# Kernel optimization log

Hardware: AMD Instinct MI355X
Metric: run time of the kernel (lower is better)

The kernel has to match this reference:

```python
import jax, jax.numpy as jnp
import numpy as np

# norse LIFParameters defaults with v_th overridden to 0.23
DT = 1e-3
TAU_SYN_INV = 200.0   # 1/5e-3
TAU_MEM_INV = 100.0   # 1/1e-2
V_TH = 0.23
ENC_V_TH = 1.0        # encoder uses default LIFParameters (v_th=1.0)
SEQ_LEN = 24
HIDDEN = 256
N_CLASSES = 10


def heaviside(x):
    return (x > 0).astype(x.dtype)


def encode(x):
    """ConstantCurrentLIFEncoder: lif_current_encoder over SEQ_LEN steps. x: [B, F] -> [T, B, F] spikes."""
    def step(v, _):
        v = v + DT * TAU_MEM_INV * (x - v)          # dv = dt*tau_mem_inv*((v_leak - v) + I)
        z = heaviside(v - ENC_V_TH)
        v = (1.0 - z) * v                            # reset to v_reset = 0
        return v, z
    _, zs = jax.lax.scan(step, jnp.zeros_like(x), None, length=SEQ_LEN)
    return zs


def lif_ff_step(inp, v, i):
    """norse lif_feed_forward_step: decay v with old i, decay i, spike, reset, then add input to i."""
    v_dec = v + DT * TAU_MEM_INV * (i - v)           # v_leak = 0
    i_dec = i * (1.0 - DT * TAU_SYN_INV)
    z = heaviside(v_dec - V_TH)
    v_new = (1.0 - z) * v_dec                        # v_reset = 0
    i_new = i_dec + inp
    return z, v_new, i_new


def setup_inputs() -> dict:
    key = jax.random.key(0)
    ks = jax.random.split(key, 8)
    B, F = 4096, 1024
    def lin(k, fan_in, fan_out):
        bound = 1.0 / np.sqrt(fan_in)
        kw, kb = jax.random.split(k)
        W = jax.random.uniform(kw, (fan_out, fan_in), jnp.float32, -bound, bound)
        b = jax.random.uniform(kb, (fan_out,), jnp.float32, -bound, bound)
        return W, b
    x = jax.random.normal(ks[0], (B, F), jnp.float32)
    W1, b1 = lin(ks[1], F, HIDDEN)
    W2, b2 = lin(ks[2], HIDDEN, HIDDEN)
    W3, b3 = lin(ks[3], HIDDEN, HIDDEN)
    Wli = jax.random.normal(ks[4], (N_CLASSES, HIDDEN), jnp.float32) * np.sqrt(2.0 / HIDDEN)
    return {"x": x, "W1": W1, "b1": b1, "W2": W2, "b2": b2, "W3": W3, "b3": b3, "Wli": Wli}


def reference(x, W1, b1, W2, b2, W3, b3, Wli):
    # dropout layers are identity in eval mode
    enc = encode(x)                                   # [T, B, F]
    B = x.shape[0]
    z2 = lambda d: jnp.zeros((B, d), x.dtype)
    carry0 = (z2(HIDDEN), z2(HIDDEN), z2(HIDDEN), z2(HIDDEN), z2(HIDDEN), z2(HIDDEN),
              z2(N_CLASSES), z2(N_CLASSES))
    def step(c, z):
        v1, i1, v2, i2, v3, i3, vo, io = c
        o1, v1, i1 = lif_ff_step(z @ W1.T + b1, v1, i1)
        o2, v2, i2 = lif_ff_step(o1 @ W2.T + b2, v2, i2)
        o2 = o2 + o1                                  # residual
        o3, v3, i3 = lif_ff_step(o2 @ W3.T + b3, v3, i3)
        o3 = o3 + o2                                  # residual
        # LILinearCell li_step: v from old i, i decays then accumulates W @ input (no bias)
        vo = vo + DT * TAU_MEM_INV * (io - vo)
        io = io * (1.0 - DT * TAU_SYN_INV) + o3 @ Wli.T
        return (v1, i1, v2, i2, v3, i3, vo, io), vo
    _, voltages = jax.lax.scan(step, carry0, enc)     # [T, B, n_classes]
    return voltages[-1]                               # decode = last timestep
```

## Files before the change

kernel.cpp:

```cpp
#include <hip/hip_runtime.h>
#include <hip/hip_bf16.h>

#define FEAT   1024
#define HID    256
#define TSTEPS 24
#define NCLS   10

typedef unsigned int u32;
typedef unsigned long long u64;
typedef unsigned short u16;
typedef float v2f __attribute__((ext_vector_type(2)));

constexpr int OFF_W1T  = 0;
constexpr int OFF_W23  = OFF_W1T + 1025*HID;
constexpr int OFF_WLI  = OFF_W23 + 257*512;
constexpr int OFF_B1   = OFF_WLI + NCLS*HID;
constexpr int OFF_B2   = OFF_B1 + HID;
constexpr int OFF_B3   = OFF_B2 + HID;

struct CoefT { float c[TSTEPS]; };
constexpr CoefT make_coef() {
    CoefT r{};
    double c = 0.0, p9 = 1.0;
    r.c[TSTEPS-1] = 0.0f;
    for (int u = TSTEPS-1; u > 0; u--) {
        c = 0.8 * c + 0.1 * p9;
        p9 *= 0.9;
        r.c[u-1] = (float)c;
    }
    return r;
}
__device__ constexpr CoefT COEF = make_coef();

__device__ __forceinline__ u32 rfl(u32 v) {
    return (u32)__builtin_amdgcn_readfirstlane((int)v);
}

__device__ __forceinline__ u32 detect_bf16(const void* __restrict__ x, u32 lane) {
    float v = __bfloat162float(((const __hip_bfloat16*)x)[lane]);
    u64 bad = __ballot(!(fabsf(v) < 100.0f));
    return bad == 0ull ? 1u : 0u;
}

__device__ __forceinline__ float rd_any(const void* p, int idx, u32 isbf) {
    return isbf ? __bfloat162float(((const __hip_bfloat16*)p)[idx])
                : ((const float*)p)[idx];
}

__device__ __forceinline__ float4 rd4(const void* p, int i, u32 isbf) {
    if (isbf) {
        const u32* q = (const u32*)p;
        u32 a = q[i >> 1], b = q[(i >> 1) + 1];
        float4 r;
        r.x = __uint_as_float(a << 16); r.y = __uint_as_float(a & 0xffff0000u);
        r.z = __uint_as_float(b << 16); r.w = __uint_as_float(b & 0xffff0000u);
        return r;
    }
    return ((const float4*)p)[i >> 2];
}

__global__ __launch_bounds__(256) void prep_k(const void* __restrict__ x,
        const void* W1, const void* W2, const void* W3, const void* Wli,
        const void* b1, const void* b2, const void* b3, float* __restrict__ ws) {
    const u32 isbf = detect_bf16(x, threadIdx.x & 63);
    const u32 t = threadIdx.x;
    int b = blockIdx.x;

    if (b == 384) {
        for (u32 e = t; e < NCLS*HID; e += 256) ws[OFF_WLI + e] = rd_any(Wli, e, isbf);
        ws[OFF_B1 + t] = rd_any(b1, t, isbf);
        ws[OFF_B2 + t] = rd_any(b2, t, isbf);
        ws[OFF_B3 + t] = rd_any(b3, t, isbf);
        ws[OFF_W1T + 1024*HID + t] = 0.f;
        ws[OFF_W23 + 256*512 + t] = 0.f;
        ws[OFF_W23 + 256*512 + 256 + t] = 0.f;
        return;
    }

    const void* src; float* dst; int srcW, dstW, coff, h0, f0;
    if (b < 256)      { src = W1; dst = ws + OFF_W1T; srcW = FEAT; dstW = HID; coff = 0;
                        h0 = (b >> 5) * 32; f0 = (b & 31) * 32; }
    else if (b < 320) { int tb = b - 256; src = W2; dst = ws + OFF_W23; srcW = HID; dstW = 512; coff = 0;
                        h0 = (tb >> 3) * 32; f0 = (tb & 7) * 32; }
    else              { int tb = b - 320; src = W3; dst = ws + OFF_W23; srcW = HID; dstW = 512; coff = 256;
                        h0 = (tb >> 3) * 32; f0 = (tb & 7) * 32; }

    __shared__ float sm[32 * 36];
    {
        u32 r = t >> 3, c4 = (t & 7) * 4;
        float4 w = rd4(src, (h0 + r) * srcW + f0 + c4, isbf);
        *(float4*)&sm[r * 36 + c4] = w;
    }
    __syncthreads();
    {
        u32 f = t >> 3, h4 = (t & 7) * 4;
        float4 o;
        o.x = sm[(h4 + 0) * 36 + f];
        o.y = sm[(h4 + 1) * 36 + f];
        o.z = sm[(h4 + 2) * 36 + f];
        o.w = sm[(h4 + 3) * 36 + f];
        *(float4*)&dst[(size_t)(f0 + f) * dstW + coff + h0 + h4] = o;
    }
}

__device__ __forceinline__ u32 mbcnt64(u64 m) {
    return __builtin_amdgcn_mbcnt_hi((u32)(m >> 32),
           __builtin_amdgcn_mbcnt_lo((u32)m, 0u));
}


__device__ __forceinline__ u32 build_listE(u16* list, u32 lm, u32 lane) {
    u32 cnt = (u32)__builtin_popcount(lm);
    u32 pos = 0, n = 0;
    #pragma unroll
    for (int b = 0; b < 5; b++) {
        u64 B = __ballot(((cnt >> b) & 1u) != 0);
        pos += mbcnt64(B) << b;
        n += ((u32)__builtin_popcountll(B)) << b;
    }
    while (lm) {
        u32 j = (u32)__builtin_ctz(lm); lm &= lm - 1;
        list[pos++] = (u16)((lane << 4) + j);
    }
    u32 np = (n + 1u) & ~1u;
    if (lane == 0 && np != n) list[n] = (u16)1024;
    return np;
}

__device__ __forceinline__ u32 build_listZ(u16* list, u32 lm, u32 start, u32 lane) {
    u32 cnt = (u32)__builtin_popcount(lm);
    u64 B0 = __ballot((cnt & 1u) != 0);
    u64 B1 = __ballot((cnt & 2u) != 0);
    u64 B2 = __ballot((cnt & 4u) != 0);
    u32 pos = start + mbcnt64(B0) + 2u*mbcnt64(B1) + 4u*mbcnt64(B2);
    u32 n = start + (u32)__builtin_popcountll(B0) + 2u*(u32)__builtin_popcountll(B1)
          + 4u*(u32)__builtin_popcountll(B2);
    while (lm) {
        u32 j = (u32)__builtin_ctz(lm); lm &= lm - 1;
        list[pos++] = (u16)((lane << 2) + j);
    }
    u32 np = (n + 1u) & ~1u;
    if (lane == 0 && np != n) list[n] = (u16)256;
    return np;
}

#define GADD(AA, BB, V) do { AA += (v2f){(V).x, (V).y}; BB += (v2f){(V).z, (V).w}; } while (0)

__device__ __forceinline__ void gather(v2f& A, v2f& B, const char* __restrict__ base,
                                       const u16* __restrict__ list, u32 np, u32 lane16,
                                       const u32 shl, const u32 disp) {
    v2f Aa = {0.f,0.f}, Ba = {0.f,0.f}, Ab = {0.f,0.f}, Bb = {0.f,0.f};
    u32 c = 0;
    for (; c + 8 <= np; c += 8) {
        uint4 d = *(const uint4*)(list + c);
        u32 w0 = rfl(d.x), w1 = rfl(d.y), w2 = rfl(d.z), w3 = rfl(d.w);
        const float4 v0 = *(const float4*)(base + ((w0 & 0xffffu) << shl) + disp + lane16);
        const float4 v1 = *(const float4*)(base + ((w0 >> 16)     << shl) + disp + lane16);
        const float4 v2 = *(const float4*)(base + ((w1 & 0xffffu) << shl) + disp + lane16);
        const float4 v3 = *(const float4*)(base + ((w1 >> 16)     << shl) + disp + lane16);
        const float4 v4 = *(const float4*)(base + ((w2 & 0xffffu) << shl) + disp + lane16);
        const float4 v5 = *(const float4*)(base + ((w2 >> 16)     << shl) + disp + lane16);
        const float4 v6 = *(const float4*)(base + ((w3 & 0xffffu) << shl) + disp + lane16);
        const float4 v7 = *(const float4*)(base + ((w3 >> 16)     << shl) + disp + lane16);
        GADD(Aa, Ba, v0); GADD(Ab, Bb, v1); GADD(Aa, Ba, v2); GADD(Ab, Bb, v3);
        GADD(Aa, Ba, v4); GADD(Ab, Bb, v5); GADD(Aa, Ba, v6); GADD(Ab, Bb, v7);
    }
    for (; c < np; c += 2) {
        u32 d = rfl(*(const u32*)(list + c));
        const float4 v0 = *(const float4*)(base + ((d & 0xffffu) << shl) + disp + lane16);
        const float4 v1 = *(const float4*)(base + ((d >> 16)     << shl) + disp + lane16);
        GADD(Aa, Ba, v0); GADD(Ab, Bb, v1);
    }
    A += Aa + Ab; B += Ba + Bb;
}

__device__ __forceinline__ void gather_dual(v2f& A2, v2f& B2, v2f& A3, v2f& B3,
        const char* __restrict__ p, const u16* __restrict__ list, u32 np, u32 lane16) {
    u32 c = 0;
    for (; c + 4 <= np; c += 4) {
        uint2 d = *(const uint2*)(list + c);
        u32 w0 = rfl(d.x), w1 = rfl(d.y);
        u32 o0 = (w0 & 0xffffu) << 11, o1 = (w0 >> 16) << 11;
        u32 o2 = (w1 & 0xffffu) << 11, o3 = (w1 >> 16) << 11;
        const float4 a0 = *(const float4*)(p + o0 + lane16);
        const float4 a1 = *(const float4*)(p + o1 + lane16);
        const float4 a2 = *(const float4*)(p + o2 + lane16);
        const float4 a3 = *(const float4*)(p + o3 + lane16);
        const float4 c0 = *(const float4*)(p + o0 + 1024 + lane16);
        const float4 c1 = *(const float4*)(p + o1 + 1024 + lane16);
        const float4 c2 = *(const float4*)(p + o2 + 1024 + lane16);
        const float4 c3 = *(const float4*)(p + o3 + 1024 + lane16);
        GADD(A2, B2, a0); GADD(A2, B2, a1); GADD(A2, B2, a2); GADD(A2, B2, a3);
        GADD(A3, B3, c0); GADD(A3, B3, c1); GADD(A3, B3, c2); GADD(A3, B3, c3);
    }
    for (; c < np; c += 2) {
        u32 d = rfl(*(const u32*)(list + c));
        u32 o0 = (d & 0xffffu) << 11, o1 = (d >> 16) << 11;
        const float4 a0 = *(const float4*)(p + o0 + lane16);
        const float4 a1 = *(const float4*)(p + o1 + lane16);
        const float4 c0 = *(const float4*)(p + o0 + 1024 + lane16);
        const float4 c1 = *(const float4*)(p + o1 + 1024 + lane16);
        GADD(A2, B2, a0); GADD(A2, B2, a1);
        GADD(A3, B3, c0); GADD(A3, B3, c1);
    }
}

__global__ __launch_bounds__(128, 4) void snn_k(const void* __restrict__ xin,
                                                const float* __restrict__ ws,
                                                void* __restrict__ out,
                                                int batch) {
    const u32 tid  = threadIdx.x;
    const u32 w    = tid >> 6;
    const u32 lane = tid & 63;
    const int row  = blockIdx.x * 2 + (int)w;
    if (row >= batch) return;
    const u32 lane16 = lane * 16;
    const u32 isbf = detect_bf16(xin, lane);

    const char* __restrict__ W1T = (const char*)(ws + OFF_W1T);
    const char* __restrict__ W23 = (const char*)(ws + OFF_W23);
    const float* __restrict__ WLI = ws + OFF_WLI;

    __shared__ u32 sched[2][12 * 64];
    __shared__ __align__(16) u16 lst[2][1024];
    u16* const lE = lst[w];
    u16* const lL = lst[w];

    {
        float xv[16];
        if (isbf) {
            const uint4* xp = (const uint4*)((const u16*)xin + (size_t)row*FEAT + lane*16);
            uint4 A = xp[0], B = xp[1];
            u32 wd[8] = {A.x, A.y, A.z, A.w, B.x, B.y, B.z, B.w};
            #pragma unroll
            for (int i = 0; i < 8; i++) {
                xv[2*i]   = __uint_as_float(wd[i] << 16);
                xv[2*i+1] = __uint_as_float(wd[i] & 0xffff0000u);
            }
        } else {
            const float4* xp = (const float4*)((const float*)xin + (size_t)row*FEAT + lane*16);
            float4 A = xp[0], B = xp[1], C = xp[2], D = xp[3];
            float tmp[16] = {A.x,A.y,A.z,A.w,B.x,B.y,B.z,B.w,C.x,C.y,C.z,C.w,D.x,D.y,D.z,D.w};
            #pragma unroll
            for (int i = 0; i < 16; i++) xv[i] = tmp[i];
        }
        u32 smreg[12];
        #pragma unroll
        for (int i = 0; i < 12; i++) smreg[i] = 0;
        #pragma unroll
        for (int j = 0; j < 16; j++) {
            float v = 0.f;
            #pragma unroll
            for (int t = 0; t < TSTEPS; t++) {
                v = v + 0.1f * (xv[j] - v);
                bool z = v > 1.0f;
                v = z ? 0.0f : v;
                if (z) smreg[t >> 1] |= 1u << (((t & 1) << 4) + j);
            }
        }
        #pragma unroll
        for (int i = 0; i < 12; i++) sched[w][i * 64 + lane] = smreg[i];
    }

    float v1[4], i1[4], v2[4], i2[4], v3[4], i3[4], g[4];
    #pragma unroll
    for (int k = 0; k < 4; k++) {
        v1[k]=0.f; i1[k]=0.f; v2[k]=0.f; i2[k]=0.f; v3[k]=0.f; i3[k]=0.f; g[k]=0.f;
    }
    const u32 lane4 = lane * 4;
    const float4 b1v = *(const float4*)(ws + OFF_B1 + lane4);
    const float4 b2v = *(const float4*)(ws + OFF_B2 + lane4);
    const float4 b3v = *(const float4*)(ws + OFF_B3 + lane4);

    u32 pairreg = 0;
    for (int t = 0; t < TSTEPS; t++) {
        if ((t & 1) == 0) pairreg = sched[w][(t >> 1) * 64 + lane];
        const u32 lmE = (t & 1) ? (pairreg >> 16) : (pairreg & 0xffffu);

        v2f accA = {b1v.x, b1v.y}, accB = {b1v.z, b1v.w};
        if (__ballot(lmE != 0u)) {
            u32 npE = build_listE(lE, lmE, lane);
            gather(accA, accB, W1T, lE, npE, lane16, 10u, 0u);
        }
        float a1[4] = {accA.x, accA.y, accB.x, accB.y};

        float o1v[4]; u32 lm1 = 0;
        #pragma unroll
        for (int kk = 0; kk < 4; kk++) {
            float vd = v1[kk] + 0.1f * (i1[kk] - v1[kk]);
            i1[kk] = i1[kk] * 0.8f;
            bool z = vd > 0.23f;
            v1[kk] = z ? 0.0f : vd;
            i1[kk] = i1[kk] + a1[kk];
            o1v[kk] = z ? 1.0f : 0.0f;
            lm1 |= (z ? 1u : 0u) << kk;
        }

        v2f acc2A = {b2v.x, b2v.y}, acc2B = {b2v.z, b2v.w};
        v2f acc3A = {b3v.x, b3v.y}, acc3B = {b3v.z, b3v.w};
        u32 np1 = 0;
        if (__ballot(lm1 != 0u)) {
            np1 = build_listZ(lL, lm1, 0u, lane);
            gather_dual(acc2A, acc2B, acc3A, acc3B, W23, lL, np1, lane16);
        }
        float a2[4] = {acc2A.x, acc2A.y, acc2B.x, acc2B.y};

        float o2v[4]; u32 lm2 = 0;
        #pragma unroll
        for (int kk = 0; kk < 4; kk++) {
            float vd = v2[kk] + 0.1f * (i2[kk] - v2[kk]);
            i2[kk] = i2[kk] * 0.8f;
            bool z = vd > 0.23f;
            v2[kk] = z ? 0.0f : vd;
            i2[kk] = i2[kk] + a2[kk];
            o2v[kk] = (z ? 1.0f : 0.0f) + o1v[kk];
            lm2 |= (z ? 1u : 0u) << kk;
        }

        if (__ballot(lm2 != 0u)) {
            u32 np2 = build_listZ(lL, lm2, np1, lane);
            gather(acc3A, acc3B, W23, lL + np1, np2 - np1, lane16, 11u, 1024u);
        }
        float a3[4] = {acc3A.x, acc3A.y, acc3B.x, acc3B.y};

        const float cf = COEF.c[t];
        #pragma unroll
        for (int kk = 0; kk < 4; kk++) {
            float vd = v3[kk] + 0.1f * (i3[kk] - v3[kk]);
            i3[kk] = i3[kk] * 0.8f;
            bool z = vd > 0.23f;
            v3[kk] = z ? 0.0f : vd;
            i3[kk] = i3[kk] + a3[kk];
            float o3 = (z ? 1.0f : 0.0f) + o2v[kk];
            g[kk] += cf * o3;
        }
    }

    float s[NCLS];
    #pragma unroll
    for (int c = 0; c < NCLS; c++) {
        const float4 wv = *(const float4*)(WLI + c*HID + lane4);
        float p = g[0]*wv.x + g[1]*wv.y + g[2]*wv.z + g[3]*wv.w;
        #pragma unroll
        for (int d = 32; d > 0; d >>= 1) p += __shfl_xor(p, d, 64);
        s[c] = p;
    }
    if (lane == 0) {
        if (isbf) {
            __hip_bfloat16* o = (__hip_bfloat16*)out + (size_t)row*NCLS;
            #pragma unroll
            for (int c = 0; c < NCLS; c++) o[c] = __float2bfloat16(s[c]);
        } else {
            float* o = (float*)out + (size_t)row*NCLS;
            #pragma unroll
            for (int c = 0; c < NCLS; c++) o[c] = s[c];
        }
    }
}

extern "C" void kernel_launch(void* const* d_in, const int* in_sizes, int n_in,
                              void* d_out, int out_size, void* d_ws, size_t ws_size,
                              hipStream_t stream) {
    const void* x   = d_in[0];
    const void* W1  = d_in[1];
    const void* b1  = d_in[2];
    const void* W2  = d_in[3];
    const void* b2  = d_in[4];
    const void* W3  = d_in[5];
    const void* b3  = d_in[6];
    const void* Wli = d_in[7];
    float* ws = (float*)d_ws;
    const int batch = in_sizes[0] / FEAT;

    prep_k<<<385, 256, 0, stream>>>(x, W1, W2, W3, Wli, b1, b2, b3, ws);
    snn_k<<<(batch + 1) / 2, 128, 0, stream>>>(x, ws, d_out, batch);
}
```

Measured before the change: 145.3 us.

## Split each batch row into producer/consumer wavefronts pipelining layer 1 against layers 2-3

Each block now handles one batch row instead of two. Wave 0 encodes the input and runs layer 1, publishing per-timestep spike masks through a shared-memory ring with a volatile flag. Wave 1 spin-waits on the flag and runs layers 2 and 3 plus the readout. The goal is to shorten the serial per-row timestep chain by overlapping layer 1 with the deeper layers, at the price of twice as many blocks, spin-waiting and possibly unbalanced work between the two waves.

```diff
diff --git a/kernel.cpp b/kernel.cpp
--- a/kernel.cpp
+++ b/kernel.cpp
@@ -212,7 +212,7 @@
     const u32 tid  = threadIdx.x;
     const u32 w    = tid >> 6;
     const u32 lane = tid & 63;
-    const int row  = blockIdx.x * 2 + (int)w;
+    const int row  = blockIdx.x;
     if (row >= batch) return;
     const u32 lane16 = lane * 16;
     const u32 isbf = detect_bf16(xin, lane);
@@ -221,139 +221,175 @@
     const char* __restrict__ W23 = (const char*)(ws + OFF_W23);
     const float* __restrict__ WLI = ws + OFF_WLI;
 
-    __shared__ u32 sched[2][12 * 64];
-    __shared__ __align__(16) u16 lst[2][1024];
-    u16* const lE = lst[w];
-    u16* const lL = lst[w];
-
-    {
-        float xv[16];
-        if (isbf) {
-            const uint4* xp = (const uint4*)((const u16*)xin + (size_t)row*FEAT + lane*16);
-            uint4 A = xp[0], B = xp[1];
-            u32 wd[8] = {A.x, A.y, A.z, A.w, B.x, B.y, B.z, B.w};
-            #pragma unroll
-            for (int i = 0; i < 8; i++) {
-                xv[2*i]   = __uint_as_float(wd[i] << 16);
-                xv[2*i+1] = __uint_as_float(wd[i] & 0xffff0000u);
-            }
-        } else {
-            const float4* xp = (const float4*)((const float*)xin + (size_t)row*FEAT + lane*16);
-            float4 A = xp[0], B = xp[1], C = xp[2], D = xp[3];
-            float tmp[16] = {A.x,A.y,A.z,A.w,B.x,B.y,B.z,B.w,C.x,C.y,C.z,C.w,D.x,D.y,D.z,D.w};
-            #pragma unroll
-            for (int i = 0; i < 16; i++) xv[i] = tmp[i];
+    __shared__ u32 sched[12 * 64];
+    __shared__ __align__(16) u16 lE[1024];
+    __shared__ __align__(16) u16 lL[768];
+    __shared__ __align__(16) u64 ring[TSTEPS][4];
+    __shared__ u32 flagv;
+
+    if (tid == 0) flagv = 0;
+    __syncthreads();
+
+    volatile u32* vf = &flagv;
+
+    if (w == 0) {
+        {
+            float xv[16];
+            if (isbf) {
+                const uint4* xp = (const uint4*)((const u16*)xin + (size_t)row*FEAT + lane*16);
+                uint4 A = xp[0], B = xp[1];
+                u32 wd[8] = {A.x, A.y, A.z, A.w, B.x, B.y, B.z, B.w};
+                #pragma unroll
+                for (int i = 0; i < 8; i++) {
+                    xv[2*i]   = __uint_as_float(wd[i] << 16);
+                    xv[2*i+1] = __uint_as_float(wd[i] & 0xffff0000u);
+                }
+            } else {
+                const float4* xp = (const float4*)((const float*)xin + (size_t)row*FEAT + lane*16);
+                float4 A = xp[0], B = xp[1], C = xp[2], D = xp[3];
+                float tmp[16] = {A.x,A.y,A.z,A.w,B.x,B.y,B.z,B.w,C.x,C.y,C.z,C.w,D.x,D.y,D.z,D.w};
+                #pragma unroll
+                for (int i = 0; i < 16; i++) xv[i] = tmp[i];
+            }
+            u32 smreg[12];
+            #pragma unroll
+            for (int i = 0; i < 12; i++) smreg[i] = 0;
+            #pragma unroll
+            for (int j = 0; j < 16; j++) {
+                float v = 0.f;
+                #pragma unroll
+                for (int t = 0; t < TSTEPS; t++) {
+                    v = v + 0.1f * (xv[j] - v);
+                    bool z = v > 1.0f;
+                    v = z ? 0.0f : v;
+                    if (z) smreg[t >> 1] |= 1u << (((t & 1) << 4) + j);
+                }
+            }
+            #pragma unroll
+            for (int i = 0; i < 12; i++) sched[i * 64 + lane] = smreg[i];
         }
-        u32 smreg[12];
+
+        float v1[4], i1[4];
         #pragma unroll
-        for (int i = 0; i < 12; i++) smreg[i] = 0;
+        for (int k = 0; k < 4; k++) { v1[k] = 0.f; i1[k] = 0.f; }
+        const float4 b1v = *(const float4*)(ws + OFF_B1 + lane * 4);
+
+        u32 pairreg = 0;
+        for (int t = 0; t < TSTEPS; t++) {
+            if ((t & 1) == 0) pairreg = sched[(t >> 1) * 64 + lane];
+            const u32 lmE = (t & 1) ? (pairreg >> 16) : (pairreg & 0xffffu);
+
+            v2f accA = {b1v.x, b1v.y}, accB = {b1v.z, b1v.w};
+            if (__ballot(lmE != 0u)) {
+                u32 npE = build_listE(lE, lmE, lane);
+                gather(accA, accB, W1T, lE, npE, lane16, 10u, 0u);
+            }
+            float a1[4] = {accA.x, accA.y, accB.x, accB.y};
+
+            u32 lm1 = 0;
+            #pragma unroll
+            for (int kk = 0; kk < 4; kk++) {
+                float vd = v1[kk] + 0.1f * (i1[kk] - v1[kk]);
+                i1[kk] = i1[kk] * 0.8f;
+                bool z = vd > 0.23f;
+                v1[kk] = z ? 0.0f : vd;
+                i1[kk] = i1[kk] + a1[kk];
+                lm1 |= (z ? 1u : 0u) << kk;
+            }
+
+            u64 m0 = __ballot((lm1 & 1u) != 0);
+            u64 m1 = __ballot((lm1 & 2u) != 0);
+            u64 m2 = __ballot((lm1 & 4u) != 0);
+            u64 m3 = __ballot((lm1 & 8u) != 0);
+            if (lane == 0) {
+                ring[t][0] = m0; ring[t][1] = m1; ring[t][2] = m2; ring[t][3] = m3;
+                __threadfence_block();
+                *vf = (u32)(t + 1);
+            }
+        }
+    } else {
+        float v2[4], i2[4], v3[4], i3[4], g[4];
         #pragma unroll
-        for (int j = 0; j < 16; j++) {
-            float v = 0.f;
-            #pragma unroll
-            for (int t = 0; t < TSTEPS; t++) {
-                v = v + 0.1f * (xv[j] - v);
-                bool z = v > 1.0f;
-                v = z ? 0.0f : v;
-                if (z) smreg[t >> 1] |= 1u << (((t & 1) << 4) + j);
+        for (int k = 0; k < 4; k++) { v2[k]=0.f; i2[k]=0.f; v3[k]=0.f; i3[k]=0.f; g[k]=0.f; }
+        const u32 lane4 = lane * 4;
+        const float4 b2v = *(const float4*)(ws + OFF_B2 + lane4);
+        const float4 b3v = *(const float4*)(ws + OFF_B3 + lane4);
+
+        u32 seen = 0;
+        for (int t = 0; t < TSTEPS; t++) {
+            if (seen < (u32)(t + 1)) {
+                do { seen = *vf; } while (seen < (u32)(t + 1));
+            }
+            __threadfence_block();
+            const volatile u64* rp = ring[t];
+            u64 m0 = rp[0], m1 = rp[1], m2 = rp[2], m3 = rp[3];
+            u32 lm1 = (u32)((m0 >> lane) & 1ull)
+                    | ((u32)((m1 >> lane) & 1ull) << 1)
+                    | ((u32)((m2 >> lane) & 1ull) << 2)
+                    | ((u32)((m3 >> lane) & 1ull) << 3);
+            float o1v[4];
+            #pragma unroll
+            for (int kk = 0; kk < 4; kk++) o1v[kk] = (lm1 >> kk) & 1u ? 1.0f : 0.0f;
+
+            v2f acc2A = {b2v.x, b2v.y}, acc2B = {b2v.z, b2v.w};
+            v2f acc3A = {b3v.x, b3v.y}, acc3B = {b3v.z, b3v.w};
+            u32 np1 = 0;
+            if (__ballot(lm1 != 0u)) {
+                np1 = build_listZ(lL, lm1, 0u, lane);
+                gather_dual(acc2A, acc2B, acc3A, acc3B, W23, lL, np1, lane16);
+            }
+            float a2[4] = {acc2A.x, acc2A.y, acc2B.x, acc2B.y};
+
+            float o2v[4]; u32 lm2 = 0;
+            #pragma unroll
+            for (int kk = 0; kk < 4; kk++) {
+                float vd = v2[kk] + 0.1f * (i2[kk] - v2[kk]);
+                i2[kk] = i2[kk] * 0.8f;
+                bool z = vd > 0.23f;
+                v2[kk] = z ? 0.0f : vd;
+                i2[kk] = i2[kk] + a2[kk];
+                o2v[kk] = (z ? 1.0f : 0.0f) + o1v[kk];
+                lm2 |= (z ? 1u : 0u) << kk;
+            }
+
+            if (__ballot(lm2 != 0u)) {
+                u32 np2 = build_listZ(lL, lm2, np1, lane);
+                gather(acc3A, acc3B, W23, lL + np1, np2 - np1, lane16, 11u, 1024u);
+            }
+            float a3[4] = {acc3A.x, acc3A.y, acc3B.x, acc3B.y};
+
+            const float cf = COEF.c[t];
+            #pragma unroll
+            for (int kk = 0; kk < 4; kk++) {
+                float vd = v3[kk] + 0.1f * (i3[kk] - v3[kk]);
+                i3[kk] = i3[kk] * 0.8f;
+                bool z = vd > 0.23f;
+                v3[kk] = z ? 0.0f : vd;
+                i3[kk] = i3[kk] + a3[kk];
+                float o3 = (z ? 1.0f : 0.0f) + o2v[kk];
+                g[kk] += cf * o3;
             }
         }
+
+        float s[NCLS];
         #pragma unroll
-        for (int i = 0; i < 12; i++) sched[w][i * 64 + lane] = smreg[i];
-    }
-
-    float v1[4], i1[4], v2[4], i2[4], v3[4], i3[4], g[4];
-    #pragma unroll
-    for (int k = 0; k < 4; k++) {
-        v1[k]=0.f; i1[k]=0.f; v2[k]=0.f; i2[k]=0.f; v3[k]=0.f; i3[k]=0.f; g[k]=0.f;
-    }
-    const u32 lane4 = lane * 4;
-    const float4 b1v = *(const float4*)(ws + OFF_B1 + lane4);
-    const float4 b2v = *(const float4*)(ws + OFF_B2 + lane4);
-    const float4 b3v = *(const float4*)(ws + OFF_B3 + lane4);
-
-    u32 pairreg = 0;
-    for (int t = 0; t < TSTEPS; t++) {
-        if ((t & 1) == 0) pairreg = sched[w][(t >> 1) * 64 + lane];
-        const u32 lmE = (t & 1) ? (pairreg >> 16) : (pairreg & 0xffffu);
-
-        v2f accA = {b1v.x, b1v.y}, accB = {b1v.z, b1v.w};
-        if (__ballot(lmE != 0u)) {
-            u32 npE = build_listE(lE, lmE, lane);
-            gather(accA, accB, W1T, lE, npE, lane16, 10u, 0u);
+        for (int c = 0; c < NCLS; c++) {
+            const float4 wv = *(const float4*)(WLI + c*HID + lane4);
+            float p = g[0]*wv.x + g[1]*wv.y + g[2]*wv.z + g[3]*wv.w;
+            #pragma unroll
+            for (int d = 32; d > 0; d >>= 1) p += __shfl_xor(p, d, 64);
+            s[c] = p;
         }
-        float a1[4] = {accA.x, accA.y, accB.x, accB.y};
-
-        float o1v[4]; u32 lm1 = 0;
-        #pragma unroll
-        for (int kk = 0; kk < 4; kk++) {
-            float vd = v1[kk] + 0.1f * (i1[kk] - v1[kk]);
-            i1[kk] = i1[kk] * 0.8f;
-            bool z = vd > 0.23f;
-            v1[kk] = z ? 0.0f : vd;
-            i1[kk] = i1[kk] + a1[kk];
-            o1v[kk] = z ? 1.0f : 0.0f;
-            lm1 |= (z ? 1u : 0u) << kk;
-        }
-
-        v2f acc2A = {b2v.x, b2v.y}, acc2B = {b2v.z, b2v.w};
-        v2f acc3A = {b3v.x, b3v.y}, acc3B = {b3v.z, b3v.w};
-        u32 np1 = 0;
-        if (__ballot(lm1 != 0u)) {
-            np1 = build_listZ(lL, lm1, 0u, lane);
-            gather_dual(acc2A, acc2B, acc3A, acc3B, W23, lL, np1, lane16);
-        }
-        float a2[4] = {acc2A.x, acc2A.y, acc2B.x, acc2B.y};
-
-        float o2v[4]; u32 lm2 = 0;
-        #pragma unroll
-        for (int kk = 0; kk < 4; kk++) {
-            float vd = v2[kk] + 0.1f * (i2[kk] - v2[kk]);
-            i2[kk] = i2[kk] * 0.8f;
-            bool z = vd > 0.23f;
-            v2[kk] = z ? 0.0f : vd;
-            i2[kk] = i2[kk] + a2[kk];
-            o2v[kk] = (z ? 1.0f : 0.0f) + o1v[kk];
-            lm2 |= (z ? 1u : 0u) << kk;
-        }
-
-        if (__ballot(lm2 != 0u)) {
-            u32 np2 = build_listZ(lL, lm2, np1, lane);
-            gather(acc3A, acc3B, W23, lL + np1, np2 - np1, lane16, 11u, 1024u);
-        }
-        float a3[4] = {acc3A.x, acc3A.y, acc3B.x, acc3B.y};
-
-        const float cf = COEF.c[t];
-        #pragma unroll
-        for (int kk = 0; kk < 4; kk++) {
-            float vd = v3[kk] + 0.1f * (i3[kk] - v3[kk]);
-            i3[kk] = i3[kk] * 0.8f;
-            bool z = vd > 0.23f;
-            v3[kk] = z ? 0.0f : vd;
-            i3[kk] = i3[kk] + a3[kk];
-            float o3 = (z ? 1.0f : 0.0f) + o2v[kk];
-            g[kk] += cf * o3;
-        }
-    }
-
-    float s[NCLS];
-    #pragma unroll
-    for (int c = 0; c < NCLS; c++) {
-        const float4 wv = *(const float4*)(WLI + c*HID + lane4);
-        float p = g[0]*wv.x + g[1]*wv.y + g[2]*wv.z + g[3]*wv.w;
-        #pragma unroll
-        for (int d = 32; d > 0; d >>= 1) p += __shfl_xor(p, d, 64);
-        s[c] = p;
-    }
-    if (lane == 0) {
-        if (isbf) {
-            __hip_bfloat16* o = (__hip_bfloat16*)out + (size_t)row*NCLS;
-            #pragma unroll
-            for (int c = 0; c < NCLS; c++) o[c] = __float2bfloat16(s[c]);
-        } else {
-            float* o = (float*)out + (size_t)row*NCLS;
-            #pragma unroll
-            for (int c = 0; c < NCLS; c++) o[c] = s[c];
+        if (lane == 0) {
+            if (isbf) {
+                __hip_bfloat16* o = (__hip_bfloat16*)out + (size_t)row*NCLS;
+                #pragma unroll
+                for (int c = 0; c < NCLS; c++) o[c] = __float2bfloat16(s[c]);
+            } else {
+                float* o = (float*)out + (size_t)row*NCLS;
+                #pragma unroll
+                for (int c = 0; c < NCLS; c++) o[c] = s[c];
+            }
         }
     }
 }
@@ -373,5 +409,5 @@
     const int batch = in_sizes[0] / FEAT;
 
     prep_k<<<385, 256, 0, stream>>>(x, W1, W2, W3, Wli, b1, b2, b3, ws);
-    snn_k<<<(batch + 1) / 2, 128, 0, stream>>>(x, ws, d_out, batch);
-}
+    snn_k<<<batch, 128, 0, stream>>>(x, ws, d_out, batch);
+}
```

New measurement: 167.3 us. 15.1% more time.

## Process SNN layers sequentially over all timesteps, pairing two timesteps per gather

Applied to the files above, without the earlier changes.

Restructures the per-row time loop into three layer-wise passes. Each pass runs all 24 timesteps for one layer and stores spike masks as packed bitmasks. Within a pass, two timesteps' spike lists are built and gathered together, so twice as many independent loads are in flight per iteration. Layer 3 now gathers W3 using both layer-1 and layer-2 spikes in one list instead of a dual W2/W3 gather. The kernel also moves from two rows per 128-thread block to one row per 64-thread block. The cost is more shared-memory list building and two list buffers per wave.

```diff
diff --git a/kernel.cpp b/kernel.cpp
--- a/kernel.cpp
+++ b/kernel.cpp
@@ -174,45 +174,51 @@
     A += Aa + Ab; B += Ba + Bb;
 }
 
-__device__ __forceinline__ void gather_dual(v2f& A2, v2f& B2, v2f& A3, v2f& B3,
-        const char* __restrict__ p, const u16* __restrict__ list, u32 np, u32 lane16) {
-    u32 c = 0;
-    for (; c + 4 <= np; c += 4) {
-        uint2 d = *(const uint2*)(list + c);
-        u32 w0 = rfl(d.x), w1 = rfl(d.y);
-        u32 o0 = (w0 & 0xffffu) << 11, o1 = (w0 >> 16) << 11;
-        u32 o2 = (w1 & 0xffffu) << 11, o3 = (w1 >> 16) << 11;
-        const float4 a0 = *(const float4*)(p + o0 + lane16);
-        const float4 a1 = *(const float4*)(p + o1 + lane16);
-        const float4 a2 = *(const float4*)(p + o2 + lane16);
-        const float4 a3 = *(const float4*)(p + o3 + lane16);
-        const float4 c0 = *(const float4*)(p + o0 + 1024 + lane16);
-        const float4 c1 = *(const float4*)(p + o1 + 1024 + lane16);
-        const float4 c2 = *(const float4*)(p + o2 + 1024 + lane16);
-        const float4 c3 = *(const float4*)(p + o3 + 1024 + lane16);
-        GADD(A2, B2, a0); GADD(A2, B2, a1); GADD(A2, B2, a2); GADD(A2, B2, a3);
-        GADD(A3, B3, c0); GADD(A3, B3, c1); GADD(A3, B3, c2); GADD(A3, B3, c3);
-    }
-    for (; c < np; c += 2) {
-        u32 d = rfl(*(const u32*)(list + c));
-        u32 o0 = (d & 0xffffu) << 11, o1 = (d >> 16) << 11;
-        const float4 a0 = *(const float4*)(p + o0 + lane16);
-        const float4 a1 = *(const float4*)(p + o1 + lane16);
-        const float4 c0 = *(const float4*)(p + o0 + 1024 + lane16);
-        const float4 c1 = *(const float4*)(p + o1 + 1024 + lane16);
-        GADD(A2, B2, a0); GADD(A2, B2, a1);
-        GADD(A3, B3, c0); GADD(A3, B3, c1);
-    }
-}
-
-__global__ __launch_bounds__(128, 4) void snn_k(const void* __restrict__ xin,
-                                                const float* __restrict__ ws,
-                                                void* __restrict__ out,
-                                                int batch) {
-    const u32 tid  = threadIdx.x;
-    const u32 w    = tid >> 6;
-    const u32 lane = tid & 63;
-    const int row  = blockIdx.x * 2 + (int)w;
+__device__ __forceinline__ void gather2(v2f& A0, v2f& B0, v2f& A1, v2f& B1,
+        const char* __restrict__ base,
+        const u16* __restrict__ la, u32 na,
+        const u16* __restrict__ lb, u32 nb,
+        u32 lane16, const u32 shl, const u32 disp) {
+    u32 ca = 0, cb = 0;
+    while (ca + 4 <= na && cb + 4 <= nb) {
+        uint2 da = *(const uint2*)(la + ca);
+        uint2 db = *(const uint2*)(lb + cb);
+        u32 wa0 = rfl(da.x), wa1 = rfl(da.y);
+        u32 wb0 = rfl(db.x), wb1 = rfl(db.y);
+        const float4 va0 = *(const float4*)(base + ((wa0 & 0xffffu) << shl) + disp + lane16);
+        const float4 va1 = *(const float4*)(base + ((wa0 >> 16)     << shl) + disp + lane16);
+        const float4 va2 = *(const float4*)(base + ((wa1 & 0xffffu) << shl) + disp + lane16);
+        const float4 va3 = *(const float4*)(base + ((wa1 >> 16)     << shl) + disp + lane16);
+        const float4 vb0 = *(const float4*)(base + ((wb0 & 0xffffu) << shl) + disp + lane16);
+        const float4 vb1 = *(const float4*)(base + ((wb0 >> 16)     << shl) + disp + lane16);
+        const float4 vb2 = *(const float4*)(base + ((wb1 & 0xffffu) << shl) + disp + lane16);
+        const float4 vb3 = *(const float4*)(base + ((wb1 >> 16)     << shl) + disp + lane16);
+        GADD(A0, B0, va0); GADD(A0, B0, va1); GADD(A0, B0, va2); GADD(A0, B0, va3);
+        GADD(A1, B1, vb0); GADD(A1, B1, vb1); GADD(A1, B1, vb2); GADD(A1, B1, vb3);
+        ca += 4; cb += 4;
+    }
+    gather(A0, B0, base, la + ca, na - ca, lane16, shl, disp);
+    gather(A1, B1, base, lb + cb, nb - cb, lane16, shl, disp);
+}
+
+#define LIF_STEP(vv, ii, aa, lmout) do {                                   \
+    lmout = 0;                                                             \
+    _Pragma("unroll")                                                      \
+    for (int kk = 0; kk < 4; kk++) {                                       \
+        float vd = vv[kk] + 0.1f * (ii[kk] - vv[kk]);                      \
+        ii[kk] = ii[kk] * 0.8f;                                            \
+        bool z = vd > 0.23f;                                               \
+        vv[kk] = z ? 0.0f : vd;                                            \
+        ii[kk] = ii[kk] + aa[kk];                                          \
+        lmout |= (z ? 1u : 0u) << kk;                                      \
+    } } while (0)
+
+__global__ __launch_bounds__(64, 4) void snn_k(const void* __restrict__ xin,
+                                               const float* __restrict__ ws,
+                                               void* __restrict__ out,
+                                               int batch) {
+    const u32 lane = threadIdx.x;
+    const int row  = blockIdx.x;
     if (row >= batch) return;
     const u32 lane16 = lane * 16;
     const u32 isbf = detect_bf16(xin, lane);
@@ -221,10 +227,9 @@
     const char* __restrict__ W23 = (const char*)(ws + OFF_W23);
     const float* __restrict__ WLI = ws + OFF_WLI;
 
-    __shared__ u32 sched[2][12 * 64];
-    __shared__ __align__(16) u16 lst[2][1024];
-    u16* const lE = lst[w];
-    u16* const lL = lst[w];
+    __shared__ u32 sched[12 * 64];
+    __shared__ __align__(16) u16 lbA[1040];
+    __shared__ __align__(16) u16 lbB[1040];
 
     {
         float xv[16];
@@ -259,83 +264,140 @@
             }
         }
         #pragma unroll
-        for (int i = 0; i < 12; i++) sched[w][i * 64 + lane] = smreg[i];
-    }
-
-    float v1[4], i1[4], v2[4], i2[4], v3[4], i3[4], g[4];
+        for (int i = 0; i < 12; i++) sched[i * 64 + lane] = smreg[i];
+    }
+
+    u32 m1[3], m2[3];
+
+    {
+        float v1[4], i1[4];
+        #pragma unroll
+        for (int k = 0; k < 4; k++) { v1[k] = 0.f; i1[k] = 0.f; }
+        const float4 b1v = *(const float4*)(ws + OFF_B1 + lane * 4);
+
+        #pragma unroll
+        for (int blk = 0; blk < 3; blk++) {
+            u32 mw = 0;
+            #pragma unroll 1
+            for (int pr = 0; pr < 4; pr++) {
+                u32 pairreg = sched[(blk*4 + pr) * 64 + lane];
+                u32 lmEa = pairreg & 0xffffu, lmEb = pairreg >> 16;
+
+                v2f aA = {b1v.x, b1v.y}, aB = {b1v.z, b1v.w};
+                v2f cA = {b1v.x, b1v.y}, cB = {b1v.z, b1v.w};
+                u32 na = 0, nb = 0;
+                if (__ballot(lmEa != 0u)) na = build_listE(lbA, lmEa, lane);
+                if (__ballot(lmEb != 0u)) nb = build_listE(lbB, lmEb, lane);
+                gather2(aA, aB, cA, cB, W1T, lbA, na, lbB, nb, lane16, 10u, 0u);
+
+                float a1a[4] = {aA.x, aA.y, aB.x, aB.y};
+                u32 lma; LIF_STEP(v1, i1, a1a, lma);
+                mw |= lma << (pr * 8);
+
+                float a1b[4] = {cA.x, cA.y, cB.x, cB.y};
+                u32 lmb; LIF_STEP(v1, i1, a1b, lmb);
+                mw |= lmb << (pr * 8 + 4);
+            }
+            m1[blk] = mw;
+        }
+    }
+
+    {
+        float v2[4], i2[4];
+        #pragma unroll
+        for (int k = 0; k < 4; k++) { v2[k] = 0.f; i2[k] = 0.f; }
+        const float4 b2v = *(const float4*)(ws + OFF_B2 + lane * 4);
+
+        #pragma unroll
+        for (int blk = 0; blk < 3; blk++) {
+            const u32 w1 = m1[blk];
+            u32 mw = 0;
+            #pragma unroll 1
+            for (int pr = 0; pr < 4; pr++) {
+                u32 lmA = (w1 >> (pr * 8)) & 0xFu;
+                u32 lmB = (w1 >> (pr * 8 + 4)) & 0xFu;
+
+                v2f aA = {b2v.x, b2v.y}, aB = {b2v.z, b2v.w};
+                v2f cA = {b2v.x, b2v.y}, cB = {b2v.z, b2v.w};
+                u32 na = 0, nb = 0;
+                if (__ballot(lmA != 0u)) na = build_listZ(lbA, lmA, 0u, lane);
+                if (__ballot(lmB != 0u)) nb = build_listZ(lbB, lmB, 0u, lane);
+                gather2(aA, aB, cA, cB, W23, lbA, na, lbB, nb, lane16, 11u, 0u);
+
+                float a2a[4] = {aA.x, aA.y, aB.x, aB.y};
+                u32 lma; LIF_STEP(v2, i2, a2a, lma);
+                mw |= lma << (pr * 8);
+
+                float a2b[4] = {cA.x, cA.y, cB.x, cB.y};
+                u32 lmb; LIF_STEP(v2, i2, a2b, lmb);
+                mw |= lmb << (pr * 8 + 4);
+            }
+            m2[blk] = mw;
+        }
+    }
+
+    float g[4];
     #pragma unroll
-    for (int k = 0; k < 4; k++) {
-        v1[k]=0.f; i1[k]=0.f; v2[k]=0.f; i2[k]=0.f; v3[k]=0.f; i3[k]=0.f; g[k]=0.f;
-    }
+    for (int k = 0; k < 4; k++) g[k] = 0.f;
+    {
+        float v3[4], i3[4];
+        #pragma unroll
+        for (int k = 0; k < 4; k++) { v3[k] = 0.f; i3[k] = 0.f; }
+        const float4 b3v = *(const float4*)(ws + OFF_B3 + lane * 4);
+
+        #pragma unroll
+        for (int blk = 0; blk < 3; blk++) {
+            const u32 w1 = m1[blk], w2 = m2[blk];
+            #pragma unroll 1
+            for (int pr = 0; pr < 4; pr++) {
+                const int t0 = blk * 8 + pr * 2;
+                u32 lmA1 = (w1 >> (pr * 8)) & 0xFu,  lmA2 = (w2 >> (pr * 8)) & 0xFu;
+                u32 lmB1 = (w1 >> (pr * 8 + 4)) & 0xFu, lmB2 = (w2 >> (pr * 8 + 4)) & 0xFu;
+
+                v2f aA = {b3v.x, b3v.y}, aB = {b3v.z, b3v.w};
+                v2f cA = {b3v.x, b3v.y}, cB = {b3v.z, b3v.w};
+                u32 na = 0, nb = 0;
+                if (__ballot(lmA1 != 0u)) na = build_listZ(lbA, lmA1, 0u, lane);
+                if (__ballot(lmA2 != 0u)) na = build_listZ(lbA, lmA2, na, lane);
+                if (__ballot(lmB1 != 0u)) nb = build_listZ(lbB, lmB1, 0u, lane);
+                if (__ballot(lmB2 != 0u)) nb = build_listZ(lbB, lmB2, nb, lane);
+                gather2(aA, aB, cA, cB, W23, lbA, na, lbB, nb, lane16, 11u, 1024u);
+
+                {
+                    float a3[4] = {aA.x, aA.y, aB.x, aB.y};
+                    const float cf = COEF.c[t0];
+                    #pragma unroll
+                    for (int kk = 0; kk < 4; kk++) {
+                        float vd = v3[kk] + 0.1f * (i3[kk] - v3[kk]);
+                        i3[kk] = i3[kk] * 0.8f;
+                        bool z = vd > 0.23f;
+                        v3[kk] = z ? 0.0f : vd;
+                        i3[kk] = i3[kk] + a3[kk];
+                        float o2 = (float)((lmA1 >> kk) & 1u) + (float)((lmA2 >> kk) & 1u);
+                        float o3 = (z ? 1.0f : 0.0f) + o2;
+                        g[kk] += cf * o3;
+                    }
+                }
+                {
+                    float a3[4] = {cA.x, cA.y, cB.x, cB.y};
+                    const float cf = COEF.c[t0 + 1];
+                    #pragma unroll
+                    for (int kk = 0; kk < 4; kk++) {
+                        float vd = v3[kk] + 0.1f * (i3[kk] - v3[kk]);
+                        i3[kk] = i3[kk] * 0.8f;
+                        bool z = vd > 0.23f;
+                        v3[kk] = z ? 0.0f : vd;
+                        i3[kk] = i3[kk] + a3[kk];
+                        float o2 = (float)((lmB1 >> kk) & 1u) + (float)((lmB2 >> kk) & 1u);
+                        float o3 = (z ? 1.0f : 0.0f) + o2;
+                        g[kk] += cf * o3;
+                    }
+                }
+            }
+        }
+    }
+
     const u32 lane4 = lane * 4;
-    const float4 b1v = *(const float4*)(ws + OFF_B1 + lane4);
-    const float4 b2v = *(const float4*)(ws + OFF_B2 + lane4);
-    const float4 b3v = *(const float4*)(ws + OFF_B3 + lane4);
-
-    u32 pairreg = 0;
-    for (int t = 0; t < TSTEPS; t++) {
-        if ((t & 1) == 0) pairreg = sched[w][(t >> 1) * 64 + lane];
-        const u32 lmE = (t & 1) ? (pairreg >> 16) : (pairreg & 0xffffu);
-
-        v2f accA = {b1v.x, b1v.y}, accB = {b1v.z, b1v.w};
-        if (__ballot(lmE != 0u)) {
-            u32 npE = build_listE(lE, lmE, lane);
-            gather(accA, accB, W1T, lE, npE, lane16, 10u, 0u);
-        }
-        float a1[4] = {accA.x, accA.y, accB.x, accB.y};
-
-        float o1v[4]; u32 lm1 = 0;
-        #pragma unroll
-        for (int kk = 0; kk < 4; kk++) {
-            float vd = v1[kk] + 0.1f * (i1[kk] - v1[kk]);
-            i1[kk] = i1[kk] * 0.8f;
-            bool z = vd > 0.23f;
-            v1[kk] = z ? 0.0f : vd;
-            i1[kk] = i1[kk] + a1[kk];
-            o1v[kk] = z ? 1.0f : 0.0f;
-            lm1 |= (z ? 1u : 0u) << kk;
-        }
-
-        v2f acc2A = {b2v.x, b2v.y}, acc2B = {b2v.z, b2v.w};
-        v2f acc3A = {b3v.x, b3v.y}, acc3B = {b3v.z, b3v.w};
-        u32 np1 = 0;
-        if (__ballot(lm1 != 0u)) {
-            np1 = build_listZ(lL, lm1, 0u, lane);
-            gather_dual(acc2A, acc2B, acc3A, acc3B, W23, lL, np1, lane16);
-        }
-        float a2[4] = {acc2A.x, acc2A.y, acc2B.x, acc2B.y};
-
-        float o2v[4]; u32 lm2 = 0;
-        #pragma unroll
-        for (int kk = 0; kk < 4; kk++) {
-            float vd = v2[kk] + 0.1f * (i2[kk] - v2[kk]);
-            i2[kk] = i2[kk] * 0.8f;
-            bool z = vd > 0.23f;
-            v2[kk] = z ? 0.0f : vd;
-            i2[kk] = i2[kk] + a2[kk];
-            o2v[kk] = (z ? 1.0f : 0.0f) + o1v[kk];
-            lm2 |= (z ? 1u : 0u) << kk;
-        }
-
-        if (__ballot(lm2 != 0u)) {
-            u32 np2 = build_listZ(lL, lm2, np1, lane);
-            gather(acc3A, acc3B, W23, lL + np1, np2 - np1, lane16, 11u, 1024u);
-        }
-        float a3[4] = {acc3A.x, acc3A.y, acc3B.x, acc3B.y};
-
-        const float cf = COEF.c[t];
-        #pragma unroll
-        for (int kk = 0; kk < 4; kk++) {
-            float vd = v3[kk] + 0.1f * (i3[kk] - v3[kk]);
-            i3[kk] = i3[kk] * 0.8f;
-            bool z = vd > 0.23f;
-            v3[kk] = z ? 0.0f : vd;
-            i3[kk] = i3[kk] + a3[kk];
-            float o3 = (z ? 1.0f : 0.0f) + o2v[kk];
-            g[kk] += cf * o3;
-        }
-    }
-
     float s[NCLS];
     #pragma unroll
     for (int c = 0; c < NCLS; c++) {
@@ -373,5 +435,5 @@
     const int batch = in_sizes[0] / FEAT;
 
     prep_k<<<385, 256, 0, stream>>>(x, W1, W2, W3, Wli, b1, b2, b3, ws);
-    snn_k<<<(batch + 1) / 2, 128, 0, stream>>>(x, ws, d_out, batch);
-}
+    snn_k<<<batch, 64, 0, stream>>>(x, ws, d_out, batch);
+}
```

Result: slower. 155.7 us (+7.2%).
